# Performance work log

Hardware: AMD Instinct MI355X
Metric: run time of the kernel (lower is better)

The kernel has to match this reference:

```python
import jax, jax.numpy as jnp
import numpy as np
from jax import lax
from jax.scipy.special import logsumexp

TEMP_MIN, TEMP_MAX = 0.1, 1.0
B, I, J, C = 2, 128, 512, 256


def setup_inputs() -> dict:
    key = jax.random.key(0)
    k1, k2, k3 = jax.random.split(key, 3)
    return {
        "text_embeddings": jax.random.normal(k1, (B, I, C), dtype=jnp.float32),
        "mel_embeddings": jax.random.normal(k2, (B, J, C), dtype=jnp.float32),
        "text_mask": jnp.ones((B, I), dtype=jnp.float32),
        "mel_mask": jnp.ones((B, J), dtype=jnp.float32),
        "noise": jax.random.gumbel(k3, (B, I, J), dtype=jnp.float32),  # -log(-log(U))
        "temperature_ratio": jnp.float32(0.5),
    }


def _cond_prob(energy, text_mask, mel_mask, direction):
    # energy: [B, I, J]; returns [B, I, J, K] log conditional probs (normalized over axis 2)
    b, i, j = energy.shape
    if direction == "alpha":
        k = j
        tri = jnp.arange(j)[:, None] >= jnp.arange(k)[None, :]  # triu(ones(J,J)).T layout -> j >= k
        mel_k = mel_mask
    else:  # beta
        k = j - 1
        tri = jnp.arange(j)[:, None] <= jnp.arange(k)[None, :]  # tril(ones(J-1,J)).T layout -> j <= k
        mel_k = mel_mask[:, :k]
    valid = (
        (text_mask[:, :, None, None] * mel_mask[:, None, :, None] * mel_k[:, None, None, :]) > 0
    ) & tri[None, None]
    e4 = jnp.where(valid, energy[..., None], -jnp.inf)  # [B,I,J,K]
    e4 = e4 - logsumexp(e4, axis=2, keepdims=True)
    return jnp.where(valid, e4, jnp.asarray(-10.0, energy.dtype))


def reference(text_embeddings, mel_embeddings, text_mask, mel_mask, noise, temperature_ratio):
    b, i_len, ct = text_embeddings.shape
    j_len, cm = mel_embeddings.shape[1], mel_embeddings.shape[2]
    ninf = jnp.asarray(-jnp.inf, text_embeddings.dtype)

    energy = jnp.einsum("bic,bjc->bij", text_embeddings, mel_embeddings) / np.sqrt(ct * cm)
    temperature = TEMP_MIN + (TEMP_MAX - TEMP_MIN) * temperature_ratio
    energy = (energy + noise) / temperature

    cpa = _cond_prob(energy, text_mask, mel_mask, "alpha")  # [B,I,J,J]
    cpb = _cond_prob(energy, text_mask, mel_mask, "beta")   # [B,I,J,J-1]

    # forward (alpha) recursion over text dim: alpha[:, i, j+1] = LSE_k(alpha[:, i-1, k] + cpa[:, i-1, j, k])
    init_a = jnp.full((b, j_len + 1), -jnp.inf, energy.dtype).at[:, 0].set(0.0)

    def astep(carry, cpa_i):  # carry [B, J+1], cpa_i [B, J, J]
        row = logsumexp(carry[:, None, :-1] + cpa_i, axis=2)  # [B, J]
        new = jnp.concatenate([jnp.full((b, 1), -jnp.inf, energy.dtype), row], axis=1)
        return new, row

    _, arows = lax.scan(astep, init_a, jnp.swapaxes(cpa, 0, 1))
    alpha = jnp.swapaxes(arows, 0, 1)  # [B, I, J] == alpha[:, 1:, 1:]

    # backward (beta) recursion: beta[:, i, j] = LSE_k(beta[:, i+1, k+1] + cpb[:, i, j, k])
    init_b = jnp.full((b, j_len), -jnp.inf, energy.dtype).at[:, -1].set(0.0)

    def bstep(carry, cpb_i):  # carry [B, J], cpb_i [B, J, J-1]
        row = logsumexp(carry[:, None, 1:] + cpb_i, axis=2)
        return row, row

    _, brows = lax.scan(bstep, init_b, jnp.flip(jnp.swapaxes(cpb[:, : i_len - 1], 0, 1), axis=0))
    beta = jnp.concatenate([jnp.flip(brows, axis=0), init_b[None]], axis=0)
    beta = jnp.swapaxes(beta, 0, 1)  # [B, I, J]

    gamma = alpha + beta
    gmask = (text_mask[:, :, None] * mel_mask[:, None, :]) > 0
    gamma = jnp.where(gmask, gamma, ninf)
    gamma = jnp.where(gmask, gamma - logsumexp(gamma, axis=1, keepdims=True), ninf)

    expanded = jnp.einsum("bij,bic->bjc", jnp.exp(gamma), text_embeddings)
    expanded = expanded * mel_mask[:, :, None]
    return gamma, expanded
```

## Files before the change

kernel.cpp:

```cpp
#include <hip/hip_runtime.h>
#include <math.h>

#define BB 2
#define II 128
#define JJ 512
#define CC 256
#define NEL (BB*II*JJ)
#define NINF (-INFINITY)
#define K10 4.5399929762484854e-5f

typedef float f32x4 __attribute__((ext_vector_type(4)));

template<int CTRL, int RM = 0xf, int BM = 0xf, bool BC = true>
__device__ __forceinline__ float dppf(float x) {
    return __int_as_float(__builtin_amdgcn_update_dpp(
        0, __float_as_int(x), CTRL, RM, BM, BC));
}
__device__ __forceinline__ float wscan_incl(float x) {
    x += dppf<0x111>(x);
    x += dppf<0x112>(x);
    x += dppf<0x114>(x);
    x += dppf<0x118>(x);
    x += dppf<0x142, 0xa>(x);
    x += dppf<0x143, 0xc>(x);
    return x;
}
__device__ __forceinline__ float lane_shr1(float x) { return dppf<0x138>(x); }
__device__ __forceinline__ float bcast63(float x) {
    return __int_as_float(__builtin_amdgcn_readlane(__float_as_int(x), 63));
}

__device__ __forceinline__ void tree_prefix8(const float x[8], float P[8]) {
    float t[8];
    t[0] = x[0];
    #pragma unroll
    for (int q = 1; q < 8; ++q) t[q] = x[q] + x[q-1];
    float u[8];
    u[0] = t[0]; u[1] = t[1];
    #pragma unroll
    for (int q = 2; q < 8; ++q) u[q] = t[q] + t[q-2];
    P[0] = u[0]; P[1] = u[1]; P[2] = u[2]; P[3] = u[3];
    #pragma unroll
    for (int q = 4; q < 8; ++q) P[q] = u[q] + u[q-4];
}

__device__ __forceinline__ void loadrow8(const float* p, float v[8]) {
    float4 a = *reinterpret_cast<const float4*>(p);
    float4 b = *reinterpret_cast<const float4*>(p + 4);
    v[0]=a.x; v[1]=a.y; v[2]=a.z; v[3]=a.w;
    v[4]=b.x; v[5]=b.y; v[6]=b.z; v[7]=b.w;
}
__device__ __forceinline__ void storerow8(float* __restrict__ p, const float v[8]) {
    *reinterpret_cast<float4*>(p)     = make_float4(v[0],v[1],v[2],v[3]);
    *reinterpret_cast<float4*>(p + 4) = make_float4(v[4],v[5],v[6],v[7]);
}

__device__ __forceinline__ void aload2(f32x4 &d0, f32x4 &d1, const float* p) {
    asm volatile("global_load_dwordx4 %0, %2, off\n\t"
                 "global_load_dwordx4 %1, %2, off offset:16"
                 : "=&v"(d0), "=&v"(d1) : "v"(p) : "memory");
}
__device__ __forceinline__ void astore2(f32x4 d0, f32x4 d1, float* p) {
    asm volatile("global_store_dwordx4 %2, %0, off\n\t"
                 "global_store_dwordx4 %2, %1, off offset:16"
                 :: "v"(d0), "v"(d1), "v"(p) : "memory");
}
template<int N> __device__ __forceinline__ void waitcnt_vm() {
    asm volatile("s_waitcnt vmcnt(%0)" :: "i"(N) : "memory");
}

struct Buf { f32x4 e0, e1, w0, w1; };

__global__ __launch_bounds__(256) void energy_kernel(
        const float* __restrict__ text, const float* __restrict__ mel,
        const float* __restrict__ noise, const float* __restrict__ ratio,
        float* __restrict__ e) {
    __shared__ float melS[64][65];
    __shared__ float texS[8][65];
    int b  = blockIdx.x;
    int i0 = blockIdx.y * 8;
    int j0 = blockIdx.z * 64;
    int t = threadIdx.x;
    int jj = t & 63, ig = t >> 6;
    float acc0 = 0.f, acc1 = 0.f;
    for (int cc = 0; cc < CC; cc += 64) {
        #pragma unroll
        for (int k = 0; k < 4; ++k) {
            int idx = t + k * 256;
            int row = idx >> 4, seg = idx & 15;
            float4 v = *reinterpret_cast<const float4*>(
                mel + (size_t)(b * JJ + j0 + row) * CC + cc + seg * 4);
            melS[row][seg*4+0] = v.x; melS[row][seg*4+1] = v.y;
            melS[row][seg*4+2] = v.z; melS[row][seg*4+3] = v.w;
        }
        if (t < 128) {
            int row = t >> 4, seg = t & 15;
            float4 v = *reinterpret_cast<const float4*>(
                text + (size_t)(b * II + i0 + row) * CC + cc + seg * 4);
            texS[row][seg*4+0] = v.x; texS[row][seg*4+1] = v.y;
            texS[row][seg*4+2] = v.z; texS[row][seg*4+3] = v.w;
        }
        __syncthreads();
        #pragma unroll 8
        for (int c = 0; c < 64; ++c) {
            float m = melS[jj][c];
            acc0 = fmaf(m, texS[ig*2+0][c], acc0);
            acc1 = fmaf(m, texS[ig*2+1][c], acc1);
        }
        __syncthreads();
    }
    float temp = 0.1f + 0.9f * ratio[0];
    float rtmp = 1.0f / temp;
    int r0 = (b * II + i0 + ig*2 + 0) * JJ + j0 + jj;
    int r1 = (b * II + i0 + ig*2 + 1) * JJ + j0 + jj;
    e[r0] = (acc0 * (1.0f/256.0f) + noise[r0]) * rtmp;
    e[r1] = (acc1 * (1.0f/256.0f) + noise[r1]) * rtmp;
}

__global__ __launch_bounds__(64) void dscan_kernel(
        const float* __restrict__ e, float* __restrict__ Ee,
        float* __restrict__ Wa, float* __restrict__ Wb) {
    int row = blockIdx.x;
    int lane = threadIdx.x;
    float v[8];
    loadrow8(e + row * JJ + lane * 8, v);
    float m = v[0];
    #pragma unroll
    for (int q = 1; q < 8; ++q) m = fmaxf(m, v[q]);
    #pragma unroll
    for (int d = 1; d < 64; d <<= 1) m = fmaxf(m, __shfl_xor(m, d, 64));
    float x[8];
    #pragma unroll
    for (int q = 0; q < 8; ++q) x[q] = __expf(v[q] - m);
    storerow8(Ee + row * JJ + lane * 8, x);
    float run = 0.f, P[8];
    #pragma unroll
    for (int q = 0; q < 8; ++q) { run += x[q]; P[q] = run; }
    float sc = wscan_incl(run);
    float cp = lane_shr1(sc);
    float run2 = 0.f, S[8];
    #pragma unroll
    for (int q = 7; q >= 0; --q) { run2 += x[q]; S[q] = run2; }
    float sd = run2;
    #pragma unroll
    for (int d = 1; d < 64; d <<= 1) { float o = __shfl_down(sd, d, 64); sd += (lane + d < 64) ? o : 0.0f; }
    float cs = __shfl_down(sd, 1, 64); if (lane == 63) cs = 0.f;
    float wa[8], wb[8];
    #pragma unroll
    for (int q = 0; q < 8; ++q) {
        wa[q] = 1.0f / (S[q] + cs);
        wb[q] = 1.0f / (P[q] + cp);
    }
    storerow8(Wa + row * JJ + lane * 8, wa);
    storerow8(Wb + row * JJ + lane * 8, wb);
}


template<bool NORM, int VM, bool PF>
__device__ __forceinline__ void astep(
    int i, int lane, int off,
    const float (&pin)[8], float (&pout)[8], float& c,
    Buf& C, Buf& L,
    const float* __restrict__ EeB, const float* __restrict__ WaB,
    float* __restrict__ paB, float* ldsC)
{
    {
        f32x4 s0 = {pin[0], pin[1], pin[2], pin[3]};
        f32x4 s1 = {pin[4], pin[5], pin[6], pin[7]};
        astore2(s0, s1, paB + (size_t)(i - 1) * JJ + off);
    }
    if (lane == 0) ldsC[i - 1] = c;
    if (PF) {
        aload2(L.e0, L.e1, EeB + (size_t)(i + 3) * JJ + off);
        aload2(L.w0, L.w1, WaB + (size_t)(i + 3) * JJ + off);
    }
    waitcnt_vm<VM>();
    __builtin_amdgcn_sched_barrier(0);
    float CE[8] = {C.e0[0],C.e0[1],C.e0[2],C.e0[3],C.e1[0],C.e1[1],C.e1[2],C.e1[3]};
    float CW[8] = {C.w0[0],C.w0[1],C.w0[2],C.w0[3],C.w1[0],C.w1[1],C.w1[2],C.w1[3]};

    float pup = lane_shr1(pin[7]);
    float y[8];
    y[0] = pup * CW[0];
    #pragma unroll
    for (int q = 1; q < 8; ++q) y[q] = pin[q-1] * CW[q];
    float zz[8];
    #pragma unroll
    for (int q = 0; q < 7; ++q) zz[q] = pin[q];
    zz[7] = (lane == 63) ? 0.0f : pin[7];
    float Y[8], Z[8];
    tree_prefix8(y, Y);
    tree_prefix8(zz, Z);
    float sy = wscan_incl(Y[7]);
    float sz = wscan_incl(Z[7]);
    float oy = lane_shr1(sy);
    float oz = lane_shr1(sz);
    float T  = bcast63(sz);
    #pragma unroll
    for (int q = 0; q < 8; ++q) {
        float S1 = oy + Y[q];
        float S2 = fmaxf(T - (oz + Z[q]) + zz[q], 0.0f);
        pout[q] = fmaf(CE[q], S1, K10 * S2);
    }
    if (NORM) {
        float Tc = fmaxf(T, 1e-30f);
        float rT = __builtin_amdgcn_rcpf(Tc);
        c += __logf(Tc);
        #pragma unroll
        for (int q = 0; q < 8; ++q) pout[q] *= rT;
    }
}

template<bool NORM, int VM, bool PF>
__device__ __forceinline__ void bstep(
    int i, int lane, int off,
    const float (&pin)[8], float (&pout)[8], float& c,
    Buf& C, Buf& L,
    const float* __restrict__ EeB, const float* __restrict__ WbB,
    float* __restrict__ pbB, float* ldsC)
{
    {
        f32x4 s0 = {pin[0], pin[1], pin[2], pin[3]};
        f32x4 s1 = {pin[4], pin[5], pin[6], pin[7]};
        astore2(s0, s1, pbB + (size_t)(i + 1) * JJ + off);
    }
    if (lane == 0) ldsC[i + 1] = c;
    if (PF) {
        aload2(L.e0, L.e1, EeB + (size_t)(i - 3) * JJ + 504 - 8 * lane);
        aload2(L.w0, L.w1, WbB + (size_t)(i - 3) * JJ + 504 - 8 * lane);
    }
    waitcnt_vm<VM>();
    __builtin_amdgcn_sched_barrier(0);
    float CE[8] = {C.e1[3],C.e1[2],C.e1[1],C.e1[0],C.e0[3],C.e0[2],C.e0[1],C.e0[0]};
    float CW[8] = {C.w1[3],C.w1[2],C.w1[1],C.w1[0],C.w0[3],C.w0[2],C.w0[1],C.w0[0]};

    float pup = lane_shr1(pin[7]);
    float pn[8];
    pn[0] = pup;
    #pragma unroll
    for (int q = 1; q < 8; ++q) pn[q] = pin[q-1];
    float w[8];
    #pragma unroll
    for (int q = 0; q < 8; ++q) w[q] = pn[q] * CW[q];
    float W[8], N[8];
    tree_prefix8(w, W);
    tree_prefix8(pn, N);
    float sw = wscan_incl(W[7]);
    float sn = wscan_incl(N[7]);
    float ow = lane_shr1(sw);
    float on = lane_shr1(sn);
    float T  = bcast63(sn);
    #pragma unroll
    for (int q = 0; q < 8; ++q) {
        float QA = ow + W[q];
        float QB = fmaxf(T - (on + N[q]), 0.0f);
        pout[q] = fmaf(CE[q], QA, K10 * QB);
    }
    if (NORM) {
        float Tc = fmaxf(T, 1e-30f);
        float rT = __builtin_amdgcn_rcpf(Tc);
        c += __logf(Tc);
        #pragma unroll
        for (int q = 0; q < 8; ++q) pout[q] *= rT;
    }
}

__global__ __launch_bounds__(64, 1) void scan_ab_kernel(
        const float* __restrict__ Ee, const float* __restrict__ Wa,
        const float* __restrict__ Wb,
        float* __restrict__ pa, float* __restrict__ pb,
        float* __restrict__ ca, float* __restrict__ cb) {
    __shared__ float ldsC[II];
    int b = blockIdx.x >> 1, dir = blockIdx.x & 1;
    int lane = threadIdx.x, off = lane * 8;
    size_t base = (size_t)b * II * JJ;
    float P0[8], P1[8], P2[8], P3[8], c = 0.0f;
    Buf B0, B1, B2, B3;

    if (dir == 0) {
        const float* EeB = Ee + base; const float* WaB = Wa + base;
        float* paB = pa + base; float* caB = ca + b * II;
        float e0r[8];
        loadrow8(EeB + off, e0r);
        float wa00 = WaB[0];
        #pragma unroll
        for (int q = 0; q < 8; ++q) P0[q] = e0r[q] * wa00;
        __builtin_amdgcn_sched_barrier(0);
        aload2(B1.e0, B1.e1, EeB + (size_t)1*JJ + off); aload2(B1.w0, B1.w1, WaB + (size_t)1*JJ + off);
        aload2(B2.e0, B2.e1, EeB + (size_t)2*JJ + off); aload2(B2.w0, B2.w1, WaB + (size_t)2*JJ + off);
        aload2(B3.e0, B3.e1, EeB + (size_t)3*JJ + off); aload2(B3.w0, B3.w1, WaB + (size_t)3*JJ + off);
        astep<true ,14,true>(1, lane, off, P0, P1, c, B1, B0, EeB, WaB, paB, ldsC);
        astep<false,16,true>(2, lane, off, P1, P2, c, B2, B1, EeB, WaB, paB, ldsC);
        #pragma unroll 1
        for (int d = 0; d < 15; ++d) {
            int ib = 3 + 8 * d;
            astep<false,18,true>(ib+0, lane, off, P2, P3, c, B3, B2, EeB, WaB, paB, ldsC);
            astep<false,18,true>(ib+1, lane, off, P3, P0, c, B0, B3, EeB, WaB, paB, ldsC);
            astep<true ,18,true>(ib+2, lane, off, P0, P1, c, B1, B0, EeB, WaB, paB, ldsC);
            astep<false,18,true>(ib+3, lane, off, P1, P2, c, B2, B1, EeB, WaB, paB, ldsC);
            astep<false,18,true>(ib+4, lane, off, P2, P3, c, B3, B2, EeB, WaB, paB, ldsC);
            astep<false,18,true>(ib+5, lane, off, P3, P0, c, B0, B3, EeB, WaB, paB, ldsC);
            astep<true ,18,true>(ib+6, lane, off, P0, P1, c, B1, B0, EeB, WaB, paB, ldsC);
            astep<false,18,true>(ib+7, lane, off, P1, P2, c, B2, B1, EeB, WaB, paB, ldsC);
        }
        astep<false,18,true >(123, lane, off, P2, P3, c, B3, B2, EeB, WaB, paB, ldsC);
        astep<false,18,true >(124, lane, off, P3, P0, c, B0, B3, EeB, WaB, paB, ldsC);
        astep<true ,14,false>(125, lane, off, P0, P1, c, B1, B0, EeB, WaB, paB, ldsC);
        astep<false,10,false>(126, lane, off, P1, P2, c, B2, B1, EeB, WaB, paB, ldsC);
        astep<false, 6,false>(127, lane, off, P2, P3, c, B3, B2, EeB, WaB, paB, ldsC);
        storerow8(paB + (size_t)127 * JJ + off, P3);
        if (lane == 0) ldsC[127] = c;
        waitcnt_vm<0>();
        caB[lane]      = ldsC[lane];
        caB[lane + 64] = ldsC[lane + 64];
    } else {
        const float* EeB = Ee + base; const float* WbB = Wb + base;
        float* pbB = pb + base; float* cbB = cb + b * II;
        #pragma unroll
        for (int q = 0; q < 8; ++q) P3[q] = 0.0f;
        P3[0] = (lane == 0) ? 1.0f : 0.0f;
        aload2(B2.e0, B2.e1, EeB + (size_t)126*JJ + 504 - 8*lane); aload2(B2.w0, B2.w1, WbB + (size_t)126*JJ + 504 - 8*lane);
        aload2(B1.e0, B1.e1, EeB + (size_t)125*JJ + 504 - 8*lane); aload2(B1.w0, B1.w1, WbB + (size_t)125*JJ + 504 - 8*lane);
        aload2(B0.e0, B0.e1, EeB + (size_t)124*JJ + 504 - 8*lane); aload2(B0.w0, B0.w1, WbB + (size_t)124*JJ + 504 - 8*lane);
        bstep<true ,14,true>(126, lane, off, P3, P2, c, B2, B3, EeB, WbB, pbB, ldsC);
        bstep<false,16,true>(125, lane, off, P2, P1, c, B1, B2, EeB, WbB, pbB, ldsC);
        #pragma unroll 1
        for (int d = 0; d < 15; ++d) {
            int ib = 124 - 8 * d;
            bstep<false,18,true>(ib-0, lane, off, P1, P0, c, B0, B1, EeB, WbB, pbB, ldsC);
            bstep<false,18,true>(ib-1, lane, off, P0, P3, c, B3, B0, EeB, WbB, pbB, ldsC);
            bstep<true ,18,true>(ib-2, lane, off, P3, P2, c, B2, B3, EeB, WbB, pbB, ldsC);
            bstep<false,18,true>(ib-3, lane, off, P2, P1, c, B1, B2, EeB, WbB, pbB, ldsC);
            bstep<false,18,true>(ib-4, lane, off, P1, P0, c, B0, B1, EeB, WbB, pbB, ldsC);
            bstep<false,18,true>(ib-5, lane, off, P0, P3, c, B3, B0, EeB, WbB, pbB, ldsC);
            bstep<true ,18,true>(ib-6, lane, off, P3, P2, c, B2, B3, EeB, WbB, pbB, ldsC);
            bstep<false,18,true>(ib-7, lane, off, P2, P1, c, B1, B2, EeB, WbB, pbB, ldsC);
        }
        bstep<false,18,true >(4, lane, off, P1, P0, c, B0, B1, EeB, WbB, pbB, ldsC);
        bstep<false,18,true >(3, lane, off, P0, P3, c, B3, B0, EeB, WbB, pbB, ldsC);
        bstep<true ,14,false>(2, lane, off, P3, P2, c, B2, B3, EeB, WbB, pbB, ldsC);
        bstep<false,10,false>(1, lane, off, P2, P1, c, B1, B2, EeB, WbB, pbB, ldsC);
        bstep<false, 6,false>(0, lane, off, P1, P0, c, B0, B1, EeB, WbB, pbB, ldsC);
        storerow8(pbB + off, P0);
        if (lane == 0) ldsC[0] = c;
        waitcnt_vm<0>();
        cbB[lane]      = ldsC[lane];
        cbB[lane + 64] = ldsC[lane + 64];
    }
}

__global__ __launch_bounds__(256) void gamma_expand_kernel(
        const float* __restrict__ pa, const float* __restrict__ pb,
        const float* __restrict__ ca, const float* __restrict__ cb,
        const float* __restrict__ text, const float* __restrict__ mmask,
        float* __restrict__ gamma_out, float* __restrict__ expanded) {
    __shared__ float wt[II][9];
    __shared__ float Ei[II];
    __shared__ float red[8][33];
    int b   = blockIdx.x >> 6;
    int jj0 = (blockIdx.x & 63) * 8;
    int t = threadIdx.x;
    int q = t & 7, ic = t >> 3;

    if (t < II) Ei[t] = ca[b*II + t] + cb[b*II + t];
    __syncthreads();
    float maxc = Ei[0];
    #pragma unroll 16
    for (int i = 1; i < II; ++i) maxc = fmaxf(maxc, Ei[i]);
    __syncthreads();
    if (t < II) Ei[t] = __expf(Ei[t] - maxc);
    __syncthreads();

    size_t idx0  = (size_t)b * II * JJ + jj0 + q;
    size_t idx0r = (size_t)b * II * JJ + (JJ - 1 - jj0 - q);
    float d = 0.f;
    #pragma unroll
    for (int k = 0; k < 4; ++k) {
        int i = ic * 4 + k;
        float P = pa[idx0 + (size_t)i * JJ] * pb[idx0r + (size_t)i * JJ] * Ei[i];
        wt[i][q] = P;
        d += P;
    }
    red[q][ic] = d;
    __syncthreads();
    if (t < 8) {
        float s = 0.f;
        #pragma unroll
        for (int k = 0; k < 32; ++k) s += red[t][k];
        red[t][32] = 1.0f / fmaxf(s, 1e-37f);
    }
    __syncthreads();
    float rD = red[q][32];
    #pragma unroll
    for (int k = 0; k < 4; ++k) {
        int i = ic * 4 + k;
        float P = wt[i][q] * rD;
        wt[i][q] = P;
        gamma_out[idx0 + (size_t)i * JJ] = fmaxf(__logf(P), -1e30f);
    }
    __syncthreads();

    float acc[8] = {0,0,0,0,0,0,0,0};
    const float* txb = text + (size_t)b * II * CC + t;
    #pragma unroll 4
    for (int i = 0; i < II; ++i) {
        float tv = txb[(size_t)i * CC];
        #pragma unroll
        for (int qq = 0; qq < 8; ++qq) acc[qq] = fmaf(wt[i][qq], tv, acc[qq]);
    }
    #pragma unroll
    for (int qq = 0; qq < 8; ++qq) {
        expanded[(size_t)(b * JJ + jj0 + qq) * CC + t] =
            acc[qq] * mmask[b * JJ + jj0 + qq];
    }
}

extern "C" void kernel_launch(void* const* d_in, const int* in_sizes, int n_in,
                              void* d_out, int out_size, void* d_ws, size_t ws_size,
                              hipStream_t stream) {
    const float* text  = (const float*)d_in[0];
    const float* mel   = (const float*)d_in[1];
    const float* mmask = (const float*)d_in[3];
    const float* noise = (const float*)d_in[4];
    const float* ratio = (const float*)d_in[5];
    float* gamma_out = (float*)d_out;
    float* expanded  = (float*)d_out + NEL;

    float* ws = (float*)d_ws;
    float* Ee = ws;
    float* Wa = ws +   NEL;
    float* Wb = ws + 2*NEL;
    float* pa = ws + 3*NEL;
    float* pb = ws + 4*NEL;
    float* ca = ws + 5*NEL;
    float* cb = ws + 5*NEL + BB*II;
    float* e  = pa;

    hipLaunchKernelGGL(energy_kernel, dim3(BB, II/8, JJ/64), dim3(256), 0, stream,
                       text, mel, noise, ratio, e);
    hipLaunchKernelGGL(dscan_kernel, dim3(BB*II), dim3(64), 0, stream, e, Ee, Wa, Wb);
    hipLaunchKernelGGL(scan_ab_kernel, dim3(BB*2), dim3(64), 0, stream,
                       Ee, Wa, Wb, pa, pb, ca, cb);
    hipLaunchKernelGGL(gamma_expand_kernel, dim3(BB*64), dim3(256), 0, stream,
                       pa, pb, ca, cb, text, mmask, gamma_out, expanded);
}
```

Baseline: 129.8 us.

## Use producer warps with LDS ring buffer to prefetch scan rows

The sequential alpha/beta scan kernel now launches 320 threads per block. Four producer wavefronts stream rows of Ee and W into a 12-deep LDS ring with global_load_lds, and the single consumer wavefront waits on per-slot flags before reading from LDS. This replaces the consumer's own register prefetch three rows ahead with a deeper producer-consumer pipeline, aiming to hide global latency on the serial critical path. It adds spin-wait polling, LDS reads on every step and cross-wave flag synchronisation that relies on volatile LDS ordering.

```diff
diff --git a/kernel.cpp b/kernel.cpp
--- a/kernel.cpp
+++ b/kernel.cpp
@@ -8,6 +8,7 @@
 #define NEL (BB*II*JJ)
 #define NINF (-INFINITY)
 #define K10 4.5399929762484854e-5f
+#define RING 12
 
 typedef float f32x4 __attribute__((ext_vector_type(4)));
 
@@ -55,11 +56,6 @@
     *reinterpret_cast<float4*>(p + 4) = make_float4(v[4],v[5],v[6],v[7]);
 }
 
-__device__ __forceinline__ void aload2(f32x4 &d0, f32x4 &d1, const float* p) {
-    asm volatile("global_load_dwordx4 %0, %2, off\n\t"
-                 "global_load_dwordx4 %1, %2, off offset:16"
-                 : "=&v"(d0), "=&v"(d1) : "v"(p) : "memory");
-}
 __device__ __forceinline__ void astore2(f32x4 d0, f32x4 d1, float* p) {
     asm volatile("global_store_dwordx4 %2, %0, off\n\t"
                  "global_store_dwordx4 %2, %1, off offset:16"
@@ -68,8 +64,11 @@
 template<int N> __device__ __forceinline__ void waitcnt_vm() {
     asm volatile("s_waitcnt vmcnt(%0)" :: "i"(N) : "memory");
 }
-
-struct Buf { f32x4 e0, e1, w0, w1; };
+typedef __attribute__((address_space(1))) float gfloat;
+typedef __attribute__((address_space(3))) float lfloat;
+__device__ __forceinline__ void gl_lds16(const float* g, float* l) {
+    __builtin_amdgcn_global_load_lds((gfloat*)g, (lfloat*)l, 16, 0, 0);
+}
 
 __global__ __launch_bounds__(256) void energy_kernel(
         const float* __restrict__ text, const float* __restrict__ mel,
@@ -156,12 +155,12 @@
 }
 
 
-template<bool NORM, int VM, bool PF>
-__device__ __forceinline__ void astep(
+template<bool NORM>
+__device__ __forceinline__ void astepL(
     int i, int lane, int off,
     const float (&pin)[8], float (&pout)[8], float& c,
-    Buf& C, Buf& L,
-    const float* __restrict__ EeB, const float* __restrict__ WaB,
+    float (*ringE)[JJ], float (*ringW)[JJ],
+    volatile int* vflg, volatile int* vdone,
     float* __restrict__ paB, float* ldsC)
 {
     {
@@ -169,15 +168,14 @@
         f32x4 s1 = {pin[4], pin[5], pin[6], pin[7]};
         astore2(s0, s1, paB + (size_t)(i - 1) * JJ + off);
     }
-    if (lane == 0) ldsC[i - 1] = c;
-    if (PF) {
-        aload2(L.e0, L.e1, EeB + (size_t)(i + 3) * JJ + off);
-        aload2(L.w0, L.w1, WaB + (size_t)(i + 3) * JJ + off);
-    }
-    waitcnt_vm<VM>();
+    if (lane == 0) { ldsC[i - 1] = c; *vdone = i - 1; }
+    int s = i % RING;
+    while (vflg[s] != i) __builtin_amdgcn_s_sleep(1);
+    waitcnt_vm<14>();
     __builtin_amdgcn_sched_barrier(0);
-    float CE[8] = {C.e0[0],C.e0[1],C.e0[2],C.e0[3],C.e1[0],C.e1[1],C.e1[2],C.e1[3]};
-    float CW[8] = {C.w0[0],C.w0[1],C.w0[2],C.w0[3],C.w1[0],C.w1[1],C.w1[2],C.w1[3]};
+    float CE[8], CW[8];
+    loadrow8(&ringE[s][off], CE);
+    loadrow8(&ringW[s][off], CW);
 
     float pup = lane_shr1(pin[7]);
     float y[8];
@@ -211,12 +209,12 @@
     }
 }
 
-template<bool NORM, int VM, bool PF>
-__device__ __forceinline__ void bstep(
+template<bool NORM>
+__device__ __forceinline__ void bstepL(
     int i, int lane, int off,
     const float (&pin)[8], float (&pout)[8], float& c,
-    Buf& C, Buf& L,
-    const float* __restrict__ EeB, const float* __restrict__ WbB,
+    float (*ringE)[JJ], float (*ringW)[JJ],
+    volatile int* vflg, volatile int* vdone,
     float* __restrict__ pbB, float* ldsC)
 {
     {
@@ -224,15 +222,17 @@
         f32x4 s1 = {pin[4], pin[5], pin[6], pin[7]};
         astore2(s0, s1, pbB + (size_t)(i + 1) * JJ + off);
     }
-    if (lane == 0) ldsC[i + 1] = c;
-    if (PF) {
-        aload2(L.e0, L.e1, EeB + (size_t)(i - 3) * JJ + 504 - 8 * lane);
-        aload2(L.w0, L.w1, WbB + (size_t)(i - 3) * JJ + 504 - 8 * lane);
-    }
-    waitcnt_vm<VM>();
+    int q126 = 126 - i;
+    if (lane == 0) { ldsC[i + 1] = c; *vdone = q126 - 1; }
+    int s = q126 % RING;
+    while (vflg[s] != q126) __builtin_amdgcn_s_sleep(1);
+    waitcnt_vm<14>();
     __builtin_amdgcn_sched_barrier(0);
-    float CE[8] = {C.e1[3],C.e1[2],C.e1[1],C.e1[0],C.e0[3],C.e0[2],C.e0[1],C.e0[0]};
-    float CW[8] = {C.w1[3],C.w1[2],C.w1[1],C.w1[0],C.w0[3],C.w0[2],C.w0[1],C.w0[0]};
+    float tE[8], tW[8], CE[8], CW[8];
+    loadrow8(&ringE[s][504 - off], tE);
+    loadrow8(&ringW[s][504 - off], tW);
+    #pragma unroll
+    for (int q = 0; q < 8; ++q) { CE[q] = tE[7-q]; CW[q] = tW[7-q]; }
 
     float pup = lane_shr1(pin[7]);
     float pn[8];
@@ -265,83 +265,125 @@
     }
 }
 
-__global__ __launch_bounds__(64, 1) void scan_ab_kernel(
+__global__ __launch_bounds__(320, 1) void scan_ab_kernel(
         const float* __restrict__ Ee, const float* __restrict__ Wa,
         const float* __restrict__ Wb,
         float* __restrict__ pa, float* __restrict__ pb,
         float* __restrict__ ca, float* __restrict__ cb) {
+    __shared__ float ringE[RING][JJ];
+    __shared__ float ringW[RING][JJ];
+    __shared__ int   flg[RING];
+    __shared__ int   done;
     __shared__ float ldsC[II];
     int b = blockIdx.x >> 1, dir = blockIdx.x & 1;
-    int lane = threadIdx.x, off = lane * 8;
+    int t = threadIdx.x;
+    int lane = t & 63, w = t >> 6;
     size_t base = (size_t)b * II * JJ;
-    float P0[8], P1[8], P2[8], P3[8], c = 0.0f;
-    Buf B0, B1, B2, B3;
+    const float* EeB = Ee + base;
+    const float* WB  = (dir == 0 ? Wa : Wb) + base;
+    volatile int* vflg  = flg;
+    volatile int* vdone = &done;
+
+    if (t < RING) flg[t] = -1;
+    if (t == RING) done = -1;
+    __syncthreads();
+
+    if (w >= 1) {
+        int nk = (dir == 0) ? 128 : 127;
+        for (int k = w - 1; k < nk; k += 4) {
+            int s = k % RING;
+            if (k >= RING) {
+                while (*vdone < k - RING) __builtin_amdgcn_s_sleep(2);
+            }
+            int row = (dir == 0) ? k : (126 - k);
+            const float* gE = EeB + (size_t)row * JJ;
+            const float* gW = WB  + (size_t)row * JJ;
+            gl_lds16(gE + lane * 4,       &ringE[s][0]);
+            gl_lds16(gE + 256 + lane * 4, &ringE[s][256]);
+            gl_lds16(gW + lane * 4,       &ringW[s][0]);
+            gl_lds16(gW + 256 + lane * 4, &ringW[s][256]);
+            waitcnt_vm<0>();
+            if (lane == 0) vflg[s] = k;
+        }
+        return;
+    }
+
+    int off = lane * 8;
+    float P0[8],P1[8],P2[8],P3[8],P4[8],P5[8],P6[8],P7[8], c = 0.0f;
 
     if (dir == 0) {
-        const float* EeB = Ee + base; const float* WaB = Wa + base;
         float* paB = pa + base; float* caB = ca + b * II;
+        while (vflg[0] != 0) __builtin_amdgcn_s_sleep(1);
         float e0r[8];
-        loadrow8(EeB + off, e0r);
-        float wa00 = WaB[0];
+        loadrow8(&ringE[0][off], e0r);
+        float wa00 = ringW[0][0];
         #pragma unroll
         for (int q = 0; q < 8; ++q) P0[q] = e0r[q] * wa00;
-        __builtin_amdgcn_sched_barrier(0);
-        aload2(B1.e0, B1.e1, EeB + (size_t)1*JJ + off); aload2(B1.w0, B1.w1, WaB + (size_t)1*JJ + off);
-        aload2(B2.e0, B2.e1, EeB + (size_t)2*JJ + off); aload2(B2.w0, B2.w1, WaB + (size_t)2*JJ + off);
-        aload2(B3.e0, B3.e1, EeB + (size_t)3*JJ + off); aload2(B3.w0, B3.w1, WaB + (size_t)3*JJ + off);
-        astep<true ,14,true>(1, lane, off, P0, P1, c, B1, B0, EeB, WaB, paB, ldsC);
-        astep<false,16,true>(2, lane, off, P1, P2, c, B2, B1, EeB, WaB, paB, ldsC);
+        astepL<true >(1, lane, off, P0, P1, c, ringE, ringW, vflg, vdone, paB, ldsC);
+        astepL<false>(2, lane, off, P1, P2, c, ringE, ringW, vflg, vdone, paB, ldsC);
+        astepL<false>(3, lane, off, P2, P3, c, ringE, ringW, vflg, vdone, paB, ldsC);
+        astepL<false>(4, lane, off, P3, P4, c, ringE, ringW, vflg, vdone, paB, ldsC);
+        astepL<true >(5, lane, off, P4, P5, c, ringE, ringW, vflg, vdone, paB, ldsC);
+        astepL<false>(6, lane, off, P5, P6, c, ringE, ringW, vflg, vdone, paB, ldsC);
+        astepL<false>(7, lane, off, P6, P7, c, ringE, ringW, vflg, vdone, paB, ldsC);
         #pragma unroll 1
-        for (int d = 0; d < 15; ++d) {
-            int ib = 3 + 8 * d;
-            astep<false,18,true>(ib+0, lane, off, P2, P3, c, B3, B2, EeB, WaB, paB, ldsC);
-            astep<false,18,true>(ib+1, lane, off, P3, P0, c, B0, B3, EeB, WaB, paB, ldsC);
-            astep<true ,18,true>(ib+2, lane, off, P0, P1, c, B1, B0, EeB, WaB, paB, ldsC);
-            astep<false,18,true>(ib+3, lane, off, P1, P2, c, B2, B1, EeB, WaB, paB, ldsC);
-            astep<false,18,true>(ib+4, lane, off, P2, P3, c, B3, B2, EeB, WaB, paB, ldsC);
-            astep<false,18,true>(ib+5, lane, off, P3, P0, c, B0, B3, EeB, WaB, paB, ldsC);
-            astep<true ,18,true>(ib+6, lane, off, P0, P1, c, B1, B0, EeB, WaB, paB, ldsC);
-            astep<false,18,true>(ib+7, lane, off, P1, P2, c, B2, B1, EeB, WaB, paB, ldsC);
-        }
-        astep<false,18,true >(123, lane, off, P2, P3, c, B3, B2, EeB, WaB, paB, ldsC);
-        astep<false,18,true >(124, lane, off, P3, P0, c, B0, B3, EeB, WaB, paB, ldsC);
-        astep<true ,14,false>(125, lane, off, P0, P1, c, B1, B0, EeB, WaB, paB, ldsC);
-        astep<false,10,false>(126, lane, off, P1, P2, c, B2, B1, EeB, WaB, paB, ldsC);
-        astep<false, 6,false>(127, lane, off, P2, P3, c, B3, B2, EeB, WaB, paB, ldsC);
-        storerow8(paB + (size_t)127 * JJ + off, P3);
+        for (int d = 0; d < 14; ++d) {
+            int i = 8 + 8 * d;
+            astepL<false>(i+0, lane, off, P7, P0, c, ringE, ringW, vflg, vdone, paB, ldsC);
+            astepL<true >(i+1, lane, off, P0, P1, c, ringE, ringW, vflg, vdone, paB, ldsC);
+            astepL<false>(i+2, lane, off, P1, P2, c, ringE, ringW, vflg, vdone, paB, ldsC);
+            astepL<false>(i+3, lane, off, P2, P3, c, ringE, ringW, vflg, vdone, paB, ldsC);
+            astepL<false>(i+4, lane, off, P3, P4, c, ringE, ringW, vflg, vdone, paB, ldsC);
+            astepL<true >(i+5, lane, off, P4, P5, c, ringE, ringW, vflg, vdone, paB, ldsC);
+            astepL<false>(i+6, lane, off, P5, P6, c, ringE, ringW, vflg, vdone, paB, ldsC);
+            astepL<false>(i+7, lane, off, P6, P7, c, ringE, ringW, vflg, vdone, paB, ldsC);
+        }
+        astepL<false>(120, lane, off, P7, P0, c, ringE, ringW, vflg, vdone, paB, ldsC);
+        astepL<true >(121, lane, off, P0, P1, c, ringE, ringW, vflg, vdone, paB, ldsC);
+        astepL<false>(122, lane, off, P1, P2, c, ringE, ringW, vflg, vdone, paB, ldsC);
+        astepL<false>(123, lane, off, P2, P3, c, ringE, ringW, vflg, vdone, paB, ldsC);
+        astepL<false>(124, lane, off, P3, P4, c, ringE, ringW, vflg, vdone, paB, ldsC);
+        astepL<true >(125, lane, off, P4, P5, c, ringE, ringW, vflg, vdone, paB, ldsC);
+        astepL<false>(126, lane, off, P5, P6, c, ringE, ringW, vflg, vdone, paB, ldsC);
+        astepL<false>(127, lane, off, P6, P7, c, ringE, ringW, vflg, vdone, paB, ldsC);
+        storerow8(paB + (size_t)127 * JJ + off, P7);
         if (lane == 0) ldsC[127] = c;
         waitcnt_vm<0>();
         caB[lane]      = ldsC[lane];
         caB[lane + 64] = ldsC[lane + 64];
     } else {
-        const float* EeB = Ee + base; const float* WbB = Wb + base;
         float* pbB = pb + base; float* cbB = cb + b * II;
         #pragma unroll
-        for (int q = 0; q < 8; ++q) P3[q] = 0.0f;
-        P3[0] = (lane == 0) ? 1.0f : 0.0f;
-        aload2(B2.e0, B2.e1, EeB + (size_t)126*JJ + 504 - 8*lane); aload2(B2.w0, B2.w1, WbB + (size_t)126*JJ + 504 - 8*lane);
-        aload2(B1.e0, B1.e1, EeB + (size_t)125*JJ + 504 - 8*lane); aload2(B1.w0, B1.w1, WbB + (size_t)125*JJ + 504 - 8*lane);
-        aload2(B0.e0, B0.e1, EeB + (size_t)124*JJ + 504 - 8*lane); aload2(B0.w0, B0.w1, WbB + (size_t)124*JJ + 504 - 8*lane);
-        bstep<true ,14,true>(126, lane, off, P3, P2, c, B2, B3, EeB, WbB, pbB, ldsC);
-        bstep<false,16,true>(125, lane, off, P2, P1, c, B1, B2, EeB, WbB, pbB, ldsC);
+        for (int q = 0; q < 8; ++q) P0[q] = 0.0f;
+        P0[0] = (lane == 0) ? 1.0f : 0.0f;
+        bstepL<true >(126, lane, off, P0, P1, c, ringE, ringW, vflg, vdone, pbB, ldsC);
+        bstepL<false>(125, lane, off, P1, P2, c, ringE, ringW, vflg, vdone, pbB, ldsC);
+        bstepL<false>(124, lane, off, P2, P3, c, ringE, ringW, vflg, vdone, pbB, ldsC);
+        bstepL<false>(123, lane, off, P3, P4, c, ringE, ringW, vflg, vdone, pbB, ldsC);
+        bstepL<true >(122, lane, off, P4, P5, c, ringE, ringW, vflg, vdone, pbB, ldsC);
+        bstepL<false>(121, lane, off, P5, P6, c, ringE, ringW, vflg, vdone, pbB, ldsC);
+        bstepL<false>(120, lane, off, P6, P7, c, ringE, ringW, vflg, vdone, pbB, ldsC);
         #pragma unroll 1
-        for (int d = 0; d < 15; ++d) {
-            int ib = 124 - 8 * d;
-            bstep<false,18,true>(ib-0, lane, off, P1, P0, c, B0, B1, EeB, WbB, pbB, ldsC);
-            bstep<false,18,true>(ib-1, lane, off, P0, P3, c, B3, B0, EeB, WbB, pbB, ldsC);
-            bstep<true ,18,true>(ib-2, lane, off, P3, P2, c, B2, B3, EeB, WbB, pbB, ldsC);
-            bstep<false,18,true>(ib-3, lane, off, P2, P1, c, B1, B2, EeB, WbB, pbB, ldsC);
-            bstep<false,18,true>(ib-4, lane, off, P1, P0, c, B0, B1, EeB, WbB, pbB, ldsC);
-            bstep<false,18,true>(ib-5, lane, off, P0, P3, c, B3, B0, EeB, WbB, pbB, ldsC);
-            bstep<true ,18,true>(ib-6, lane, off, P3, P2, c, B2, B3, EeB, WbB, pbB, ldsC);
-            bstep<false,18,true>(ib-7, lane, off, P2, P1, c, B1, B2, EeB, WbB, pbB, ldsC);
-        }
-        bstep<false,18,true >(4, lane, off, P1, P0, c, B0, B1, EeB, WbB, pbB, ldsC);
-        bstep<false,18,true >(3, lane, off, P0, P3, c, B3, B0, EeB, WbB, pbB, ldsC);
-        bstep<true ,14,false>(2, lane, off, P3, P2, c, B2, B3, EeB, WbB, pbB, ldsC);
-        bstep<false,10,false>(1, lane, off, P2, P1, c, B1, B2, EeB, WbB, pbB, ldsC);
-        bstep<false, 6,false>(0, lane, off, P1, P0, c, B0, B1, EeB, WbB, pbB, ldsC);
-        storerow8(pbB + off, P0);
+        for (int d = 0; d < 14; ++d) {
+            int i = 119 - 8 * d;
+            bstepL<false>(i-0, lane, off, P7, P0, c, ringE, ringW, vflg, vdone, pbB, ldsC);
+            bstepL<true >(i-1, lane, off, P0, P1, c, ringE, ringW, vflg, vdone, pbB, ldsC);
+            bstepL<false>(i-2, lane, off, P1, P2, c, ringE, ringW, vflg, vdone, pbB, ldsC);
+            bstepL<false>(i-3, lane, off, P2, P3, c, ringE, ringW, vflg, vdone, pbB, ldsC);
+            bstepL<false>(i-4, lane, off, P3, P4, c, ringE, ringW, vflg, vdone, pbB, ldsC);
+            bstepL<true >(i-5, lane, off, P4, P5, c, ringE, ringW, vflg, vdone, pbB, ldsC);
+            bstepL<false>(i-6, lane, off, P5, P6, c, ringE, ringW, vflg, vdone, pbB, ldsC);
+            bstepL<false>(i-7, lane, off, P6, P7, c, ringE, ringW, vflg, vdone, pbB, ldsC);
+        }
+        bstepL<false>(7, lane, off, P7, P0, c, ringE, ringW, vflg, vdone, pbB, ldsC);
+        bstepL<true >(6, lane, off, P0, P1, c, ringE, ringW, vflg, vdone, pbB, ldsC);
+        bstepL<false>(5, lane, off, P1, P2, c, ringE, ringW, vflg, vdone, pbB, ldsC);
+        bstepL<false>(4, lane, off, P2, P3, c, ringE, ringW, vflg, vdone, pbB, ldsC);
+        bstepL<false>(3, lane, off, P3, P4, c, ringE, ringW, vflg, vdone, pbB, ldsC);
+        bstepL<true >(2, lane, off, P4, P5, c, ringE, ringW, vflg, vdone, pbB, ldsC);
+        bstepL<false>(1, lane, off, P5, P6, c, ringE, ringW, vflg, vdone, pbB, ldsC);
+        bstepL<false>(0, lane, off, P6, P7, c, ringE, ringW, vflg, vdone, pbB, ldsC);
+        storerow8(pbB + off, P7);
         if (lane == 0) ldsC[0] = c;
         waitcnt_vm<0>();
         cbB[lane]      = ldsC[lane];
@@ -439,7 +481,7 @@
     hipLaunchKernelGGL(energy_kernel, dim3(BB, II/8, JJ/64), dim3(256), 0, stream,
                        text, mel, noise, ratio, e);
     hipLaunchKernelGGL(dscan_kernel, dim3(BB*II), dim3(64), 0, stream, e, Ee, Wa, Wb);
-    hipLaunchKernelGGL(scan_ab_kernel, dim3(BB*2), dim3(64), 0, stream,
+    hipLaunchKernelGGL(scan_ab_kernel, dim3(BB*2), dim3(320), 0, stream,
                        Ee, Wa, Wb, pa, pb, ca, cb);
     hipLaunchKernelGGL(gamma_expand_kernel, dim3(BB*64), dim3(256), 0, stream,
                        pa, pb, ca, cb, text, mmask, gamma_out, expanded);
```

New measurement: 155.8 us. +20.1%, slower.
